# Optimization experiments

Measured on AMD Instinct MI355X. Metric: run time of the kernel, lower is better.

## Reference

```python
import jax, jax.numpy as jnp
import numpy as np

P = 16  # patch_size


def setup_inputs() -> dict:
    key = jax.random.key(0)
    k1, k2 = jax.random.split(key)
    B, N, C = 128, P * P, 768
    x = jax.random.normal(k1, (B, N, C), dtype=jnp.float32)
    # learned spectral filter: (P, P//2+1, C, 2) real/imag pairs, init ~ N(0, 0.02^2)
    complex_weight = jax.random.normal(k2, (P, P // 2 + 1, C, 2), dtype=jnp.float32) * 0.02
    return {"x": x, "complex_weight": complex_weight}


def reference(x, complex_weight):
    dtype = x.dtype
    xf = x.astype(jnp.float32)
    B, N, C = xf.shape
    xf = xf.reshape(B, P, P, C)
    # 2D real FFT over spatial dims with orthonormal scaling -> [B, P, P//2+1, C] complex
    Xf = jnp.fft.rfft2(xf, axes=(1, 2), norm="ortho")
    weight = jax.lax.complex(complex_weight[..., 0], complex_weight[..., 1])  # [P, P//2+1, C]
    Xf = Xf * weight  # broadcast over batch
    out = jnp.fft.irfft2(Xf, s=(P, P), axes=(1, 2), norm="ortho")
    return out.reshape(B, N, C).astype(dtype)
```

## Files before the change

kernel.cpp:

```cpp
#include <hip/hip_runtime.h>


constexpr int PP = 16;
constexpr int NS = 256;
constexpr int CH = 768;
constexpr int NB = 128;

__global__ void gf_build_k(const float* __restrict__ w, float* __restrict__ kbuf) {
    const int pq = blockIdx.x;
    const int c  = blockIdx.y * blockDim.x + threadIdx.x;
    const int p = pq >> 4, q = pq & 15;

    float ct[16], st[16];
#pragma unroll
    for (int t = 0; t < 16; ++t) {
        const float ang = 6.28318530717958647692f * (float)t * (1.0f / 16.0f);
        ct[t] = cosf(ang);
        st[t] = sinf(ang);
    }

    float acc = 0.0f;
#pragma unroll
    for (int u = 0; u < 16; ++u) {
#pragma unroll
        for (int v = 0; v <= 8; ++v) {
            const float cv = (v == 0 || v == 8) ? 1.0f : 2.0f;
            const int t = (u * p + v * q) & 15;
            const float* wp = w + 2 * ((size_t)((u * 9 + v) * CH) + c);
            acc += cv * (wp[0] * ct[t] - wp[1] * st[t]);
        }
    }
    kbuf[pq * CH + c] = acc * (1.0f / 256.0f);
}

__global__ __launch_bounds__(128) void gf_conv(const float* __restrict__ x,
                                               const float* __restrict__ kbuf,
                                               float* __restrict__ out) {
    __shared__ __align__(16) float xs[NS][32];
    const int b   = blockIdx.y;
    const int c0  = blockIdx.x * 32;
    const int tid = threadIdx.x;

    {
        const int ch4 = (tid & 7) << 2;
        const int sr  = tid >> 3;
        const float* xb = x + (size_t)b * NS * CH + c0;
#pragma unroll
        for (int i = 0; i < 16; ++i) {
            const int s = (i << 4) + sr;
            *(float4*)&xs[s][ch4] = *(const float4*)(xb + (size_t)s * CH + ch4);
        }
    }
    __syncthreads();

    const int ch = (tid & 7) << 2;
    const int n  = tid >> 3;

    float4 acc[16];
#pragma unroll
    for (int m = 0; m < 16; ++m) acc[m] = make_float4(0.f, 0.f, 0.f, 0.f);

    const float* kb = kbuf + c0 + ch;

#pragma unroll 1
    for (int qq = 0; qq < 16; ++qq) {
        const int q = (qq + n) & 15;
        const int j = (n - q) & 15;

        float4 xv[16];
#pragma unroll
        for (int r = 0; r < 16; ++r)
            xv[r] = *(const float4*)&xs[(r << 4) + j][ch];

#pragma unroll
        for (int p = 0; p < 16; ++p) {
            const float4 kv = *(const float4*)(kb + (size_t)(((p << 4) | q)) * CH);
#pragma unroll
            for (int m = 0; m < 16; ++m) {
                const float4 xx = xv[(m - p) & 15];
                acc[m].x = fmaf(kv.x, xx.x, acc[m].x);
                acc[m].y = fmaf(kv.y, xx.y, acc[m].y);
                acc[m].z = fmaf(kv.z, xx.z, acc[m].z);
                acc[m].w = fmaf(kv.w, xx.w, acc[m].w);
            }
        }
    }

    float* ob = out + (size_t)b * NS * CH + c0 + ch;
#pragma unroll
    for (int m = 0; m < 16; ++m)
        *(float4*)(ob + (size_t)((m << 4) + n) * CH) = acc[m];
}

extern "C" void kernel_launch(void* const* d_in, const int* in_sizes, int n_in,
                              void* d_out, int out_size, void* d_ws, size_t ws_size,
                              hipStream_t stream) {
    const float* x = (const float*)d_in[0];
    const float* w = (const float*)d_in[1];
    float* out  = (float*)d_out;
    float* kbuf = (float*)d_ws;

    gf_build_k<<<dim3(256, 3), 256, 0, stream>>>(w, kbuf);
    gf_conv<<<dim3(CH / 32, NB), 128, 0, stream>>>(x, kbuf, out);
}
```

Measured before the change: 320.3 us.

## Stage filter kernel in LDS and halve channel tile for more parallelism

```diff
diff --git a/kernel.cpp b/kernel.cpp
--- a/kernel.cpp
+++ b/kernel.cpp
@@ -5,19 +5,21 @@
 constexpr int NS = 256;
 constexpr int CH = 768;
 constexpr int NB = 128;
+constexpr int CB = 16;
+constexpr int XS = 20;
 
 __global__ void gf_build_k(const float* __restrict__ w, float* __restrict__ kbuf) {
+    __shared__ float ct[16], st[16];
+    if (threadIdx.x < 16) {
+        const float ang = 6.28318530717958647692f * (float)threadIdx.x * (1.0f / 16.0f);
+        ct[threadIdx.x] = cosf(ang);
+        st[threadIdx.x] = sinf(ang);
+    }
+    __syncthreads();
+
     const int pq = blockIdx.x;
     const int c  = blockIdx.y * blockDim.x + threadIdx.x;
     const int p = pq >> 4, q = pq & 15;
-
-    float ct[16], st[16];
-#pragma unroll
-    for (int t = 0; t < 16; ++t) {
-        const float ang = 6.28318530717958647692f * (float)t * (1.0f / 16.0f);
-        ct[t] = cosf(ang);
-        st[t] = sinf(ang);
-    }
 
     float acc = 0.0f;
 #pragma unroll
@@ -33,38 +35,40 @@
     kbuf[pq * CH + c] = acc * (1.0f / 256.0f);
 }
 
-__global__ __launch_bounds__(128) void gf_conv(const float* __restrict__ x,
-                                               const float* __restrict__ kbuf,
-                                               float* __restrict__ out) {
-    __shared__ __align__(16) float xs[NS][32];
+__global__ __launch_bounds__(128, 2) void gf_conv(const float* __restrict__ x,
+                                                  const float* __restrict__ kbuf,
+                                                  float* __restrict__ out) {
+    __shared__ __align__(16) float xs[NS][XS];
+    __shared__ __align__(16) float ks[NS][CB];
+
     const int b   = blockIdx.y;
-    const int c0  = blockIdx.x * 32;
+    const int c0  = blockIdx.x * CB;
     const int tid = threadIdx.x;
 
     {
-        const int ch4 = (tid & 7) << 2;
-        const int sr  = tid >> 3;
         const float* xb = x + (size_t)b * NS * CH + c0;
+        const float* kb = kbuf + c0;
 #pragma unroll
-        for (int i = 0; i < 16; ++i) {
-            const int s = (i << 4) + sr;
-            *(float4*)&xs[s][ch4] = *(const float4*)(xb + (size_t)s * CH + ch4);
+        for (int i = 0; i < 8; ++i) {
+            const int T  = i * 128 + tid;
+            const int s  = T >> 2;
+            const int g4 = (T & 3) << 2;
+            *(float4*)&xs[s][g4] = *(const float4*)(xb + (size_t)s * CH + g4);
+            *(float4*)&ks[s][g4] = *(const float4*)(kb + (size_t)s * CH + g4);
         }
     }
     __syncthreads();
 
-    const int ch = (tid & 7) << 2;
-    const int n  = tid >> 3;
+    const int ch = (tid & 3) << 2;
+    const int n  = (tid >> 2) & 15;
+    const int mb = (tid >> 6) << 3;
 
-    float4 acc[16];
+    float4 acc[8];
 #pragma unroll
-    for (int m = 0; m < 16; ++m) acc[m] = make_float4(0.f, 0.f, 0.f, 0.f);
-
-    const float* kb = kbuf + c0 + ch;
+    for (int m = 0; m < 8; ++m) acc[m] = make_float4(0.f, 0.f, 0.f, 0.f);
 
 #pragma unroll 1
-    for (int qq = 0; qq < 16; ++qq) {
-        const int q = (qq + n) & 15;
+    for (int q = 0; q < 16; ++q) {
         const int j = (n - q) & 15;
 
         float4 xv[16];
@@ -74,10 +78,10 @@
 
 #pragma unroll
         for (int p = 0; p < 16; ++p) {
-            const float4 kv = *(const float4*)(kb + (size_t)(((p << 4) | q)) * CH);
+            const float4 kv = *(const float4*)&ks[(p << 4) + q][ch];
 #pragma unroll
-            for (int m = 0; m < 16; ++m) {
-                const float4 xx = xv[(m - p) & 15];
+            for (int m = 0; m < 8; ++m) {
+                const float4 xx = xv[(mb + m - p) & 15];
                 acc[m].x = fmaf(kv.x, xx.x, acc[m].x);
                 acc[m].y = fmaf(kv.y, xx.y, acc[m].y);
                 acc[m].z = fmaf(kv.z, xx.z, acc[m].z);
@@ -88,8 +92,8 @@
 
     float* ob = out + (size_t)b * NS * CH + c0 + ch;
 #pragma unroll
-    for (int m = 0; m < 16; ++m)
-        *(float4*)(ob + (size_t)((m << 4) + n) * CH) = acc[m];
+    for (int m = 0; m < 8; ++m)
+        *(float4*)(ob + (size_t)(((mb + m) << 4) + n) * CH) = acc[m];
 }
 
 extern "C" void kernel_launch(void* const* d_in, const int* in_sizes, int n_in,
@@ -101,5 +105,5 @@
     float* kbuf = (float*)d_ws;
 
     gf_build_k<<<dim3(256, 3), 256, 0, stream>>>(w, kbuf);
-    gf_conv<<<dim3(CH / 32, NB), 128, 0, stream>>>(x, kbuf, out);
+    gf_conv<<<dim3(CH / CB, NB), 128, 0, stream>>>(x, kbuf, out);
 }
```

Measured after the change: 1.087 ms. 239% more time.
